# Optimization experiments

Hardware: AMD Instinct MI355X
Metric: run time of the kernel (lower is better)

Reference implementation:

```python
import jax, jax.numpy as jnp
from jax import lax
import numpy as np

GAMMA = 0.25  # bottleneck commitment-loss weight (bn.gamma)
B, Q, N = 8, 64, 8192
K = 512       # n_quant_vecs (codebook size)
C = 256       # n_classes (mu-law quantization levels)


def setup_inputs() -> dict:
    key = jax.random.key(0)
    k1, k2, k3, k4 = jax.random.split(key, 4)
    ze = jax.random.normal(k1, (B, Q, N), dtype=jnp.float32)
    emb = jax.random.normal(k2, (K, Q), dtype=jnp.float32)
    quant_pred = jax.random.normal(k3, (B, C, N), dtype=jnp.float32)
    target_wav = jax.random.randint(k4, (B, N), 0, C, dtype=jnp.int64)
    return {"ze": ze, "emb": emb, "quant_pred": quant_pred, "target_wav": target_wav}


def reference(ze, emb, quant_pred, target_wav):
    # --- VQ codebook nearest-neighbor squared L2 distance ---
    # Original materializes (B,K,Q,N) diff; we use the expansion
    # ||z-e||^2 = ||z||^2 + ||e||^2 - 2 z.e to avoid the huge intermediate.
    ze2 = jnp.sum(ze * ze, axis=1)                       # (B,N)
    emb2 = jnp.sum(emb * emb, axis=1)                    # (K,)
    dots = jnp.einsum('bqn,kq->bkn', ze, emb)            # (B,K,N)
    d = ze2[:, None, :] + emb2[None, :, None] - 2.0 * dots  # (B,K,N)
    kmin = jnp.argmin(lax.stop_gradient(d), axis=1)      # (B,N)
    e_sel = emb[kmin]                                    # (B,N,Q) selected codewords
    ze_t = jnp.transpose(ze, (0, 2, 1))                  # (B,N,Q)

    # l2 loss: sg(ze) vs emb  -> gradient flows to codebook only
    l2_loss = jnp.sum((lax.stop_gradient(ze_t) - e_sel) ** 2, axis=-1)       # (B,N)
    # commitment loss: bn.min_dist uses sg(emb) -> gradient flows to ze only
    com_loss = GAMMA * jnp.sum((ze_t - lax.stop_gradient(e_sel)) ** 2, axis=-1)  # (B,N)

    # --- reconstruction CE: log-softmax over class dim + gather target ---
    log_pred = jax.nn.log_softmax(quant_pred, axis=1)    # (B,C,N)
    lp_t = jnp.take_along_axis(log_pred, target_wav[:, None, :], axis=1)[:, 0, :]  # (B,N)
    rec_loss = -lp_t

    total_loss = rec_loss.sum() + l2_loss.sum() + com_loss.sum()
    return total_loss
```

## Files before the change

kernel.cpp:

```cpp
#include <hip/hip_runtime.h>
#include <math.h>

#define GAMMA 0.25f
constexpr int B_ = 8, Q_ = 64, N_ = 8192, K_ = 512, C_ = 256;

typedef __attribute__((ext_vector_type(8))) short bf16x8;
typedef __attribute__((ext_vector_type(4))) short short4v;
typedef __attribute__((ext_vector_type(4))) float f32x4;

static __device__ inline short f2bf(float x) {
    union { float f; unsigned u; } v; v.f = x;
    unsigned r = (v.u + 0x7fffu + ((v.u >> 16) & 1u)) >> 16;
    return (short)r;
}
static __device__ inline float bf2f(short h) {
    union { unsigned u; float f; } v; v.u = ((unsigned)(unsigned short)h) << 16;
    return v.f;
}

__global__ __launch_bounds__(256) void prep_kernel(const float* __restrict__ emb,
                                                   short* __restrict__ embB,
                                                   float* __restrict__ e2g)
{
    const int r = blockIdx.x * 256 + threadIdx.x;
    if (r >= K_) return;
    const float4* src = (const float4*)(emb + r * Q_);
    short4v* dst = (short4v*)(embB + r * Q_);
    float s = 0.f;
    #pragma unroll
    for (int i = 0; i < 16; ++i) {
        const float4 v = src[i];
        short4v h;
        h[0] = f2bf(v.x); h[1] = f2bf(v.y); h[2] = f2bf(v.z); h[3] = f2bf(v.w);
        dst[i] = h;
        #pragma unroll
        for (int j = 0; j < 4; ++j) { const float a = bf2f(h[j]); s = fmaf(a, a, s); }
    }
    e2g[r] = s;
}

__global__ __launch_bounds__(256) void mega_kernel(
    const float* __restrict__ ze, const float* __restrict__ qp,
    const int* __restrict__ tgt, const short* __restrict__ embB,
    const float* __restrict__ e2g,
    float* __restrict__ cePart, float* __restrict__ vqPart)
{
    __shared__ f32x4 sh4[(64 * 68 + 256) / 4];
    const int bid  = blockIdx.x;
    const int tid  = threadIdx.x;
    const int lane = tid & 63;
    const int w    = tid >> 6;

    if (bid % 3 != 0) {
        const int cbid = bid - bid / 3 - 1;
        f32x4* parts = sh4;

        const int g    = lane & 7;
        const int c0   = lane >> 3;

        const int base = cbid * 32;
        const int b    = base >> 13;
        const int n0   = base & (N_ - 1);
        const float* qpb = qp + (size_t)b * C_ * N_;
        const float* qpn = qpb + n0 + g * 4;
        const int cbase  = w * 64 + c0 * 8;

        float4 v[8];
        #pragma unroll
        for (int j = 0; j < 8; ++j)
            v[j] = *(const float4*)(qpn + (size_t)(cbase + j) * N_);

        float xts[4] = {0.f, 0.f, 0.f, 0.f};
        if ((w == 0) && (lane < 8)) {
            #pragma unroll
            for (int j = 0; j < 4; ++j) {
                const int t = tgt[base + lane * 4 + j];
                xts[j] = qpb[(size_t)t * N_ + n0 + lane * 4 + j];
            }
        }

        f32x4 acc = {0.f, 0.f, 0.f, 0.f};
        #pragma unroll
        for (int j = 0; j < 8; ++j) {
            acc[0] += __expf(v[j].x); acc[1] += __expf(v[j].y);
            acc[2] += __expf(v[j].z); acc[3] += __expf(v[j].w);
        }
        #pragma unroll
        for (int r = 0; r < 4; ++r) {
            acc[r] += __shfl_xor(acc[r], 8, 64);
            acc[r] += __shfl_xor(acc[r], 16, 64);
            acc[r] += __shfl_xor(acc[r], 32, 64);
        }
        if (c0 == 0) parts[w * 8 + g] = acc;
        __syncthreads();

        if (w == 0) {
            float loss = 0.f;
            if (lane < 8) {
                const f32x4 tot = (parts[lane] + parts[8 + lane]) +
                                  (parts[16 + lane] + parts[24 + lane]);
                #pragma unroll
                for (int j = 0; j < 4; ++j) loss += __logf(tot[j]) - xts[j];
            }
            loss += __shfl_down(loss, 4, 64);
            loss += __shfl_down(loss, 2, 64);
            loss += __shfl_down(loss, 1, 64);
            if (lane == 0) cePart[cbid] = loss;
        }
    } else {
        const int vbid = bid / 3;
        float* smem = (float*)sh4;
        float* minb = smem + 64 * 68;

        const int n16  = lane & 15;
        const int quad = lane >> 4;

        const int base = vbid * 64;
        const int b    = base >> 13;
        const int n0   = base & (N_ - 1);
        const float* zb = ze + (size_t)b * Q_ * N_;

        const int q  = tid >> 2;
        const int pt = tid & 3;
        const float* zq = zb + (size_t)q * N_ + n0 + pt * 4;
        float4 st[4];
        #pragma unroll
        for (int i = 0; i < 4; ++i)
            st[i] = *(const float4*)(zq + i * 16);

        const short* bb = embB + (w * 128 + n16) * Q_ + quad * 8;
        bf16x8 Bv[8][2];
        float  e2v[8];
        #pragma unroll
        for (int t = 0; t < 8; ++t) {
            Bv[t][0] = *(const bf16x8*)(bb + t * 16 * Q_);
            Bv[t][1] = *(const bf16x8*)(bb + t * 16 * Q_ + 32);
            e2v[t]   = e2g[w * 128 + t * 16 + n16];
        }

        #pragma unroll
        for (int i = 0; i < 4; ++i) {
            const int nn = i * 16 + pt * 4;
            smem[(nn + 0) * 68 + q] = st[i].x;
            smem[(nn + 1) * 68 + q] = st[i].y;
            smem[(nn + 2) * 68 + q] = st[i].z;
            smem[(nn + 3) * 68 + q] = st[i].w;
        }
        __syncthreads();

        bf16x8 afrag[4][2];
        float zsq = 0.f;
        #pragma unroll
        for (int u = 0; u < 4; ++u) {
            #pragma unroll
            for (int s = 0; s < 2; ++s) {
                const float* bse = smem + (u * 16 + n16) * 68 + s * 32 + quad * 8;
                const f32x4 x0 = *(const f32x4*)(bse);
                const f32x4 x1 = *(const f32x4*)(bse + 4);
                #pragma unroll
                for (int j = 0; j < 4; ++j) {
                    zsq = fmaf(x0[j], x0[j], zsq);
                    afrag[u][s][j] = f2bf(-2.f * x0[j]);
                }
                #pragma unroll
                for (int j = 0; j < 4; ++j) {
                    zsq = fmaf(x1[j], x1[j], zsq);
                    afrag[u][s][4 + j] = f2bf(-2.f * x1[j]);
                }
            }
        }

        f32x4 best[4];
        #pragma unroll
        for (int u = 0; u < 4; ++u) best[u] = (f32x4){1e30f, 1e30f, 1e30f, 1e30f};

        #pragma unroll
        for (int t = 0; t < 8; ++t) {
            const f32x4 ce2 = {e2v[t], e2v[t], e2v[t], e2v[t]};
            #pragma unroll
            for (int u = 0; u < 4; ++u) {
                f32x4 a = __builtin_amdgcn_mfma_f32_16x16x32_bf16(afrag[u][0], Bv[t][0], ce2, 0, 0, 0);
                a       = __builtin_amdgcn_mfma_f32_16x16x32_bf16(afrag[u][1], Bv[t][1], a,   0, 0, 0);
                #pragma unroll
                for (int r = 0; r < 4; ++r) best[u][r] = fminf(best[u][r], a[r]);
            }
        }

        #pragma unroll
        for (int m = 1; m < 16; m <<= 1) {
            #pragma unroll
            for (int u = 0; u < 4; ++u) {
                #pragma unroll
                for (int r = 0; r < 4; ++r)
                    best[u][r] = fminf(best[u][r], __shfl_xor(best[u][r], m, 64));
            }
        }
        if (n16 == 0) {
            #pragma unroll
            for (int u = 0; u < 4; ++u) {
                #pragma unroll
                for (int r = 0; r < 4; ++r)
                    minb[w * 64 + u * 16 + quad * 4 + r] = best[u][r];
            }
        }
        __syncthreads();

        if (w == 0) {
            const float mn = fminf(fminf(minb[lane], minb[64 + lane]),
                                   fminf(minb[128 + lane], minb[192 + lane]));
            float val = 1.25f * (mn + zsq);
            #pragma unroll
            for (int off = 32; off > 0; off >>= 1) val += __shfl_down(val, off, 64);
            if (lane == 0) vqPart[vbid] = val;
        }
    }
}

__global__ __launch_bounds__(256) void reduce_kernel(const float* __restrict__ cePart,
                                                     const float* __restrict__ vqPart,
                                                     float* __restrict__ out)
{
    __shared__ float sm[4];
    const int tid = threadIdx.x;
    float s = 0.f;
    #pragma unroll
    for (int i = 0; i < 8; ++i) s += cePart[tid + i * 256];
    #pragma unroll
    for (int i = 0; i < 4; ++i) s += vqPart[tid + i * 256];
    #pragma unroll
    for (int off = 32; off > 0; off >>= 1) s += __shfl_down(s, off, 64);
    if ((tid & 63) == 0) sm[tid >> 6] = s;
    __syncthreads();
    if (tid == 0) out[0] = (sm[0] + sm[1]) + (sm[2] + sm[3]);
}

extern "C" void kernel_launch(void* const* d_in, const int* in_sizes, int n_in,
                              void* d_out, int out_size, void* d_ws, size_t ws_size,
                              hipStream_t stream) {
    const float* ze  = (const float*)d_in[0];
    const float* emb = (const float*)d_in[1];
    const float* qp  = (const float*)d_in[2];
    const int*   tgt = (const int*)d_in[3];
    float* out = (float*)d_out;

    short* embB   = (short*)d_ws;
    float* e2g    = (float*)((char*)d_ws + 65536);
    float* cePart = (float*)((char*)d_ws + 65536 + 2048);
    float* vqPart = (float*)((char*)d_ws + 65536 + 2048 + 8192);

    prep_kernel<<<2, 256, 0, stream>>>(emb, embB, e2g);
    mega_kernel<<<3072, 256, 0, stream>>>(ze, qp, tgt, embB, e2g, cePart, vqPart);
    reduce_kernel<<<1, 256, 0, stream>>>(cePart, vqPart, out);
}
```

Baseline: 123.2 us.

## Coarsen mega_kernel blocks with double-buffered loads for CE and VQ paths

Cuts the grid from 3072 small blocks to 512. Each CE block now covers 256 positions and each VQ block 256 positions. Inside each block the next tile's global loads (qp rows, ze tiles) are issued before the current tile is computed, with a second LDS buffer for ze. This loads the codebook fragments and e2 once per block rather than per 64 positions and shrinks the partial-sum array. The trade-off is fewer blocks than a 256-CU part can comfortably spread work across (256 CE plus 256 VQ blocks), plus more registers and LDS per block, which may lower occupancy and latency hiding.

```diff
diff --git a/kernel.cpp b/kernel.cpp
--- a/kernel.cpp
+++ b/kernel.cpp
@@ -45,84 +45,89 @@
     const float* __restrict__ e2g,
     float* __restrict__ cePart, float* __restrict__ vqPart)
 {
-    __shared__ f32x4 sh4[(64 * 68 + 256) / 4];
+    __shared__ f32x4 sh4[2432];
     const int bid  = blockIdx.x;
     const int tid  = threadIdx.x;
     const int lane = tid & 63;
     const int w    = tid >> 6;
 
-    if (bid % 3 != 0) {
-        const int cbid = bid - bid / 3 - 1;
-        f32x4* parts = sh4;
-
-        const int g    = lane & 7;
-        const int c0   = lane >> 3;
-
-        const int base = cbid * 32;
-        const int b    = base >> 13;
-        const int n0   = base & (N_ - 1);
+    if (bid < 256) {
+        f32x4* ceparts = sh4;
+        float* xb      = (float*)(sh4 + 256);
+
+        const int base0 = bid * 256;
+        const int b     = base0 >> 13;
+        const int n0    = base0 & (N_ - 1);
         const float* qpb = qp + (size_t)b * C_ * N_;
+
+        const int tg = tgt[base0 + tid];
+        const float xval = qpb[(size_t)tg * N_ + n0 + tid];
+
+        const int g  = lane & 7;
+        const int c0 = lane >> 3;
+        const int cbase = w * 64 + c0 * 8;
         const float* qpn = qpb + n0 + g * 4;
-        const int cbase  = w * 64 + c0 * 8;
-
-        float4 v[8];
+
+        float4 v[2][8];
         #pragma unroll
         for (int j = 0; j < 8; ++j)
-            v[j] = *(const float4*)(qpn + (size_t)(cbase + j) * N_);
-
-        float xts[4] = {0.f, 0.f, 0.f, 0.f};
-        if ((w == 0) && (lane < 8)) {
-            #pragma unroll
-            for (int j = 0; j < 4; ++j) {
-                const int t = tgt[base + lane * 4 + j];
-                xts[j] = qpb[(size_t)t * N_ + n0 + lane * 4 + j];
-            }
-        }
-
-        f32x4 acc = {0.f, 0.f, 0.f, 0.f};
-        #pragma unroll
-        for (int j = 0; j < 8; ++j) {
-            acc[0] += __expf(v[j].x); acc[1] += __expf(v[j].y);
-            acc[2] += __expf(v[j].z); acc[3] += __expf(v[j].w);
-        }
-        #pragma unroll
-        for (int r = 0; r < 4; ++r) {
-            acc[r] += __shfl_xor(acc[r], 8, 64);
-            acc[r] += __shfl_xor(acc[r], 16, 64);
-            acc[r] += __shfl_xor(acc[r], 32, 64);
-        }
-        if (c0 == 0) parts[w * 8 + g] = acc;
+            v[0][j] = *(const float4*)(qpn + (size_t)(cbase + j) * N_);
+
+        #pragma unroll
+        for (int t = 0; t < 8; ++t) {
+            if (t < 7) {
+                #pragma unroll
+                for (int j = 0; j < 8; ++j)
+                    v[(t + 1) & 1][j] = *(const float4*)(qpn + (t + 1) * 32 +
+                                                         (size_t)(cbase + j) * N_);
+            }
+            f32x4 acc = {0.f, 0.f, 0.f, 0.f};
+            #pragma unroll
+            for (int j = 0; j < 8; ++j) {
+                const float4 x = v[t & 1][j];
+                acc[0] += __expf(x.x); acc[1] += __expf(x.y);
+                acc[2] += __expf(x.z); acc[3] += __expf(x.w);
+            }
+            #pragma unroll
+            for (int r = 0; r < 4; ++r) {
+                acc[r] += __shfl_xor(acc[r], 8, 64);
+                acc[r] += __shfl_xor(acc[r], 16, 64);
+                acc[r] += __shfl_xor(acc[r], 32, 64);
+            }
+            if (c0 == 0) ceparts[t * 32 + w * 8 + g] = acc;
+        }
+        xb[tid] = xval;
         __syncthreads();
 
-        if (w == 0) {
+        if (tid < 64) {
+            const int t = tid >> 3, gg = tid & 7;
+            const f32x4 tot = (ceparts[t * 32 + gg] + ceparts[t * 32 + 8 + gg]) +
+                              (ceparts[t * 32 + 16 + gg] + ceparts[t * 32 + 24 + gg]);
             float loss = 0.f;
-            if (lane < 8) {
-                const f32x4 tot = (parts[lane] + parts[8 + lane]) +
-                                  (parts[16 + lane] + parts[24 + lane]);
-                #pragma unroll
-                for (int j = 0; j < 4; ++j) loss += __logf(tot[j]) - xts[j];
-            }
-            loss += __shfl_down(loss, 4, 64);
-            loss += __shfl_down(loss, 2, 64);
-            loss += __shfl_down(loss, 1, 64);
-            if (lane == 0) cePart[cbid] = loss;
+            #pragma unroll
+            for (int j = 0; j < 4; ++j)
+                loss += __logf(tot[j]) - xb[t * 32 + gg * 4 + j];
+            #pragma unroll
+            for (int off = 32; off > 0; off >>= 1) loss += __shfl_down(loss, off, 64);
+            if (tid == 0) cePart[bid] = loss;
         }
     } else {
-        const int vbid = bid / 3;
-        float* smem = (float*)sh4;
-        float* minb = smem + 64 * 68;
+        const int vbid  = bid - 256;
+        float* zebuf0 = (float*)sh4;
+        float* zebuf1 = zebuf0 + 64 * 68;
+        float* minb   = zebuf0 + 2 * 64 * 68;
 
         const int n16  = lane & 15;
         const int quad = lane >> 4;
-
-        const int base = vbid * 64;
-        const int b    = base >> 13;
-        const int n0   = base & (N_ - 1);
+        const int base0 = vbid * 256;
+        const int b     = base0 >> 13;
+        const int n0    = base0 & (N_ - 1);
         const float* zb = ze + (size_t)b * Q_ * N_;
 
         const int q  = tid >> 2;
         const int pt = tid & 3;
         const float* zq = zb + (size_t)q * N_ + n0 + pt * 4;
+
         float4 st[4];
         #pragma unroll
         for (int i = 0; i < 4; ++i)
@@ -141,77 +146,104 @@
         #pragma unroll
         for (int i = 0; i < 4; ++i) {
             const int nn = i * 16 + pt * 4;
-            smem[(nn + 0) * 68 + q] = st[i].x;
-            smem[(nn + 1) * 68 + q] = st[i].y;
-            smem[(nn + 2) * 68 + q] = st[i].z;
-            smem[(nn + 3) * 68 + q] = st[i].w;
+            zebuf0[(nn + 0) * 68 + q] = st[i].x;
+            zebuf0[(nn + 1) * 68 + q] = st[i].y;
+            zebuf0[(nn + 2) * 68 + q] = st[i].z;
+            zebuf0[(nn + 3) * 68 + q] = st[i].w;
         }
         __syncthreads();
 
-        bf16x8 afrag[4][2];
-        float zsq = 0.f;
-        #pragma unroll
-        for (int u = 0; u < 4; ++u) {
-            #pragma unroll
-            for (int s = 0; s < 2; ++s) {
-                const float* bse = smem + (u * 16 + n16) * 68 + s * 32 + quad * 8;
-                const f32x4 x0 = *(const f32x4*)(bse);
-                const f32x4 x1 = *(const f32x4*)(bse + 4);
-                #pragma unroll
-                for (int j = 0; j < 4; ++j) {
-                    zsq = fmaf(x0[j], x0[j], zsq);
-                    afrag[u][s][j] = f2bf(-2.f * x0[j]);
-                }
-                #pragma unroll
-                for (int j = 0; j < 4; ++j) {
-                    zsq = fmaf(x1[j], x1[j], zsq);
-                    afrag[u][s][4 + j] = f2bf(-2.f * x1[j]);
-                }
-            }
-        }
-
-        f32x4 best[4];
-        #pragma unroll
-        for (int u = 0; u < 4; ++u) best[u] = (f32x4){1e30f, 1e30f, 1e30f, 1e30f};
-
-        #pragma unroll
-        for (int t = 0; t < 8; ++t) {
-            const f32x4 ce2 = {e2v[t], e2v[t], e2v[t], e2v[t]};
+        float zs[4];
+        #pragma unroll
+        for (int t = 0; t < 4; ++t) {
+            float* bufc = (t & 1) ? zebuf1 : zebuf0;
+            float* bufn = (t & 1) ? zebuf0 : zebuf1;
+
+            if (t < 3) {
+                #pragma unroll
+                for (int i = 0; i < 4; ++i)
+                    st[i] = *(const float4*)(zq + (t + 1) * 64 + i * 16);
+            }
+
+            bf16x8 afrag[4][2];
+            float zsq = 0.f;
             #pragma unroll
             for (int u = 0; u < 4; ++u) {
-                f32x4 a = __builtin_amdgcn_mfma_f32_16x16x32_bf16(afrag[u][0], Bv[t][0], ce2, 0, 0, 0);
-                a       = __builtin_amdgcn_mfma_f32_16x16x32_bf16(afrag[u][1], Bv[t][1], a,   0, 0, 0);
-                #pragma unroll
-                for (int r = 0; r < 4; ++r) best[u][r] = fminf(best[u][r], a[r]);
-            }
-        }
-
-        #pragma unroll
-        for (int m = 1; m < 16; m <<= 1) {
-            #pragma unroll
-            for (int u = 0; u < 4; ++u) {
-                #pragma unroll
-                for (int r = 0; r < 4; ++r)
-                    best[u][r] = fminf(best[u][r], __shfl_xor(best[u][r], m, 64));
-            }
-        }
-        if (n16 == 0) {
-            #pragma unroll
-            for (int u = 0; u < 4; ++u) {
-                #pragma unroll
-                for (int r = 0; r < 4; ++r)
-                    minb[w * 64 + u * 16 + quad * 4 + r] = best[u][r];
-            }
-        }
-        __syncthreads();
+                #pragma unroll
+                for (int s = 0; s < 2; ++s) {
+                    const float* bse = bufc + (u * 16 + n16) * 68 + s * 32 + quad * 8;
+                    const f32x4 x0 = *(const f32x4*)(bse);
+                    const f32x4 x1 = *(const f32x4*)(bse + 4);
+                    #pragma unroll
+                    for (int j = 0; j < 4; ++j) {
+                        zsq = fmaf(x0[j], x0[j], zsq);
+                        afrag[u][s][j] = f2bf(-2.f * x0[j]);
+                    }
+                    #pragma unroll
+                    for (int j = 0; j < 4; ++j) {
+                        zsq = fmaf(x1[j], x1[j], zsq);
+                        afrag[u][s][4 + j] = f2bf(-2.f * x1[j]);
+                    }
+                }
+            }
+            zs[t] = zsq;
+
+            f32x4 best[4];
+            #pragma unroll
+            for (int u = 0; u < 4; ++u) best[u] = (f32x4){1e30f, 1e30f, 1e30f, 1e30f};
+            #pragma unroll
+            for (int tt = 0; tt < 8; ++tt) {
+                const f32x4 ce2 = {e2v[tt], e2v[tt], e2v[tt], e2v[tt]};
+                #pragma unroll
+                for (int u = 0; u < 4; ++u) {
+                    f32x4 a = __builtin_amdgcn_mfma_f32_16x16x32_bf16(afrag[u][0], Bv[tt][0], ce2, 0, 0, 0);
+                    a       = __builtin_amdgcn_mfma_f32_16x16x32_bf16(afrag[u][1], Bv[tt][1], a,   0, 0, 0);
+                    #pragma unroll
+                    for (int r = 0; r < 4; ++r) best[u][r] = fminf(best[u][r], a[r]);
+                }
+            }
+            #pragma unroll
+            for (int m = 1; m < 16; m <<= 1) {
+                #pragma unroll
+                for (int u = 0; u < 4; ++u) {
+                    #pragma unroll
+                    for (int r = 0; r < 4; ++r)
+                        best[u][r] = fminf(best[u][r], __shfl_xor(best[u][r], m, 64));
+                }
+            }
+            if (n16 == 0) {
+                #pragma unroll
+                for (int u = 0; u < 4; ++u) {
+                    #pragma unroll
+                    for (int r = 0; r < 4; ++r)
+                        minb[t * 256 + w * 64 + u * 16 + quad * 4 + r] = best[u][r];
+                }
+            }
+
+            if (t < 3) {
+                #pragma unroll
+                for (int i = 0; i < 4; ++i) {
+                    const int nn = i * 16 + pt * 4;
+                    bufn[(nn + 0) * 68 + q] = st[i].x;
+                    bufn[(nn + 1) * 68 + q] = st[i].y;
+                    bufn[(nn + 2) * 68 + q] = st[i].z;
+                    bufn[(nn + 3) * 68 + q] = st[i].w;
+                }
+            }
+            __syncthreads();
+        }
 
         if (w == 0) {
-            const float mn = fminf(fminf(minb[lane], minb[64 + lane]),
-                                   fminf(minb[128 + lane], minb[192 + lane]));
-            float val = 1.25f * (mn + zsq);
-            #pragma unroll
-            for (int off = 32; off > 0; off >>= 1) val += __shfl_down(val, off, 64);
-            if (lane == 0) vqPart[vbid] = val;
+            float vsum = 0.f;
+            #pragma unroll
+            for (int t = 0; t < 4; ++t) {
+                const float mn = fminf(fminf(minb[t * 256 + lane], minb[t * 256 + 64 + lane]),
+                                       fminf(minb[t * 256 + 128 + lane], minb[t * 256 + 192 + lane]));
+                vsum += 1.25f * (mn + zs[t]);
+            }
+            #pragma unroll
+            for (int off = 32; off > 0; off >>= 1) vsum += __shfl_down(vsum, off, 64);
+            if (lane == 0) vqPart[vbid] = vsum;
         }
     }
 }
@@ -222,11 +254,7 @@
 {
     __shared__ float sm[4];
     const int tid = threadIdx.x;
-    float s = 0.f;
-    #pragma unroll
-    for (int i = 0; i < 8; ++i) s += cePart[tid + i * 256];
-    #pragma unroll
-    for (int i = 0; i < 4; ++i) s += vqPart[tid + i * 256];
+    float s = cePart[tid] + vqPart[tid];
     #pragma unroll
     for (int off = 32; off > 0; off >>= 1) s += __shfl_down(s, off, 64);
     if ((tid & 63) == 0) sm[tid >> 6] = s;
@@ -245,10 +273,10 @@
 
     short* embB   = (short*)d_ws;
     float* e2g    = (float*)((char*)d_ws + 65536);
-    float* cePart = (float*)((char*)d_ws + 65536 + 2048);
-    float* vqPart = (float*)((char*)d_ws + 65536 + 2048 + 8192);
+    float* cePart = (float*)((char*)d_ws + 67584);
+    float* vqPart = (float*)((char*)d_ws + 68608);
 
     prep_kernel<<<2, 256, 0, stream>>>(emb, embB, e2g);
-    mega_kernel<<<3072, 256, 0, stream>>>(ze, qp, tgt, embB, e2g, cePart, vqPart);
+    mega_kernel<<<512, 256, 0, stream>>>(ze, qp, tgt, embB, e2g, cePart, vqPart);
     reduce_kernel<<<1, 256, 0, stream>>>(cePart, vqPart, out);
 }
```

Measured after the change: 125.0 us. About the same (+1.4%).
